# Performance work log

Hardware: AMD Instinct MI355X
Metric: run time of the kernel (lower is better)

## Reference

```python
import jax, jax.numpy as jnp
import numpy as np

B, IS, D = 16, 56, 768
NH, HD = 12, 64
WS = 14
MLP = 3072
EPS = 1e-5


def layer_norm(x, g, b):
    mu = jnp.mean(x, axis=-1, keepdims=True)
    var = jnp.mean(jnp.square(x - mu), axis=-1, keepdims=True)
    return (x - mu) * jax.lax.rsqrt(var + EPS) * g + b


def window_partition(x, ws):
    b, h, w, c = x.shape
    x = x.reshape(b, h // ws, ws, w // ws, ws, c)
    return x.transpose(0, 1, 3, 2, 4, 5).reshape(-1, ws, ws, c)


def window_unpartition(windows, ws, h, w, b):
    c = windows.shape[-1]
    x = windows.reshape(b, h // ws, w // ws, ws, ws, c)
    return x.transpose(0, 1, 3, 2, 4, 5).reshape(b, h, w, c)


def get_rel_pos(q_size, k_size, rel_pos):
    # q_size == k_size == WS here, table already has 2*WS-1 rows (no resize)
    coords = jnp.arange(q_size)[:, None] - jnp.arange(k_size)[None, :] + (k_size - 1)
    return rel_pos[coords]  # (q, k, hd)


def attention(x, qkv_w, qkv_b, proj_w, proj_b, rel_pos_h, rel_pos_w):
    b, h, w, d = x.shape
    scale = HD ** -0.5
    qkv = x @ qkv_w + qkv_b                                  # (b,h,w,3D)
    qkv = qkv.reshape(b, h * w, 3, NH, HD).transpose(2, 0, 3, 1, 4)
    qkv = qkv.reshape(3, b * NH, h * w, HD)
    q, k, v = qkv[0], qkv[1], qkv[2]
    attn = jnp.einsum('bqc,bkc->bqk', q * scale, k)          # (b*NH, hw, hw)
    # decomposed relative position bias
    rh = get_rel_pos(h, h, rel_pos_h)                        # (h,h,HD)
    rw = get_rel_pos(w, w, rel_pos_w)                        # (w,w,HD)
    r_q = q.reshape(b * NH, h, w, HD)
    rel_h = jnp.einsum('bhwc,hkc->bhwk', r_q, rh)
    rel_w = jnp.einsum('bhwc,wkc->bhwk', r_q, rw)
    attn = (attn.reshape(b * NH, h, w, h, w)
            + rel_h[:, :, :, :, None] + rel_w[:, :, :, None, :])
    attn = attn.reshape(b * NH, h * w, h * w)
    attn = jax.nn.softmax(attn, axis=-1)
    out = attn @ v                                           # (b*NH, hw, HD)
    out = out.reshape(b, NH, h, w, HD).transpose(0, 2, 3, 1, 4).reshape(b, h, w, d)
    return out @ proj_w + proj_b


def setup_inputs() -> dict:
    key = jax.random.key(0)
    ks = jax.random.split(key, 12)
    s = lambda fan_in: 1.0 / np.sqrt(fan_in)
    return {
        'x': jax.random.normal(ks[0], (B, IS, IS, D), jnp.float32),
        'norm1_g': jnp.ones((D,), jnp.float32),
        'norm1_b': jnp.zeros((D,), jnp.float32),
        'qkv_w': jax.random.normal(ks[1], (D, 3 * D), jnp.float32) * s(D),
        'qkv_b': jnp.zeros((3 * D,), jnp.float32),
        'proj_w': jax.random.normal(ks[2], (D, D), jnp.float32) * s(D),
        'proj_b': jnp.zeros((D,), jnp.float32),
        'rel_pos_h': jax.random.normal(ks[3], (2 * WS - 1, HD), jnp.float32) * 0.02,
        'rel_pos_w': jax.random.normal(ks[4], (2 * WS - 1, HD), jnp.float32) * 0.02,
        'norm2_g': jnp.ones((D,), jnp.float32),
        'norm2_b': jnp.zeros((D,), jnp.float32),
        'lin1_w': jax.random.normal(ks[5], (D, MLP), jnp.float32) * s(D),
        'lin1_b': jnp.zeros((MLP,), jnp.float32),
        'lin2_w': jax.random.normal(ks[6], (MLP, D), jnp.float32) * s(MLP),
        'lin2_b': jnp.zeros((D,), jnp.float32),
    }


def reference(x, norm1_g, norm1_b, qkv_w, qkv_b, proj_w, proj_b,
              rel_pos_h, rel_pos_w, norm2_g, norm2_b,
              lin1_w, lin1_b, lin2_w, lin2_b):
    b, h, w, d = x.shape
    shortcut = x
    xn = layer_norm(x, norm1_g, norm1_b)
    x_win = window_partition(xn, WS)
    attn_out = attention(x_win, qkv_w, qkv_b, proj_w, proj_b, rel_pos_h, rel_pos_w)
    attn_res = window_unpartition(attn_out, WS, h, w, b)
    hidden = shortcut + attn_res
    normed = layer_norm(hidden, norm2_g, norm2_b)
    m = jax.nn.gelu(normed.reshape(b, h * w, d) @ lin1_w + lin1_b, approximate=False)
    mlp_out = (m @ lin2_w + lin2_b).reshape(b, h, w, d)
    return hidden + mlp_out
```

## Files before the change

kernel.cpp:

```cpp
#include <hip/hip_runtime.h>
#include <cstdint>
#include <cstddef>


typedef unsigned short u16;
typedef __attribute__((ext_vector_type(8))) short bf16x8;
typedef __attribute__((ext_vector_type(4))) short bf16x4;
typedef __attribute__((ext_vector_type(4))) float f32x4;

#define MFMA16(a,b,c) __builtin_amdgcn_mfma_f32_16x16x32_bf16(a,b,c,0,0,0)

__device__ __forceinline__ float bf2f(u16 u){
  union { unsigned int i; float f; } v; v.i = ((unsigned int)u) << 16; return v.f;
}
__device__ __forceinline__ u16 f2bf(float f){
  union { float f; unsigned int i; } v; v.f = f;
  unsigned int r = v.i + 0x7FFFu + ((v.i >> 16) & 1u);
  return (u16)(r >> 16);
}
__device__ __forceinline__ f32x4 f4zero(){ f32x4 z; z[0]=z[1]=z[2]=z[3]=0.f; return z; }
__device__ __forceinline__ bf16x8 ld8(const u16* p){ return *reinterpret_cast<const bf16x8*>(p); }

__device__ __forceinline__ void gld_lds16(const u16* g, u16* l){
  __builtin_amdgcn_global_load_lds(
      (const __attribute__((address_space(1))) unsigned int*)(g),
      (__attribute__((address_space(3))) unsigned int*)(l), 16, 0, 0);
}

__global__ __launch_bounds__(256)
void conv_transpose(const float* __restrict__ in, u16* __restrict__ out, int R, int C)
{
  __shared__ float tile[32][33];
  int cb = C >> 5;
  int bx = blockIdx.x % cb, by = blockIdx.x / cb;
  int c0 = bx << 5, r0 = by << 5;
  int tx = threadIdx.x & 31, ty = threadIdx.x >> 5;
  #pragma unroll
  for (int k = 0; k < 4; k++)
    tile[ty + 8*k][tx] = in[(size_t)(r0 + ty + 8*k) * C + c0 + tx];
  __syncthreads();
  #pragma unroll
  for (int k = 0; k < 4; k++)
    out[(size_t)(c0 + ty + 8*k) * R + r0 + tx] = f2bf(tile[tx][ty + 8*k]);
}

__global__ __launch_bounds__(256)
void conv_bf16(const float* __restrict__ a, const float* __restrict__ b,
               u16* __restrict__ oa, u16* __restrict__ ob, int n)
{
  int i = blockIdx.x * 256 + threadIdx.x;
  if (i < n){ oa[i] = f2bf(a[i]); ob[i] = f2bf(b[i]); }
}

__global__ __launch_bounds__(256)
void ln_kernel(const float* __restrict__ in, const float* __restrict__ g,
               const float* __restrict__ b, u16* __restrict__ out, int window_map)
{
  const int wv = threadIdx.x >> 6, lane = threadIdx.x & 63;
  const int token = blockIdx.x * 4 + wv;
  const float* row = in + (size_t)token * 768;
  float vals[12];
  float s = 0.f, s2 = 0.f;
  #pragma unroll
  for (int j = 0; j < 3; j++){
    float4 u = *reinterpret_cast<const float4*>(row + j*256 + lane*4);
    float t[4] = {u.x, u.y, u.z, u.w};
    #pragma unroll
    for (int e = 0; e < 4; e++){ vals[j*4+e] = t[e]; s += t[e]; s2 += t[e]*t[e]; }
  }
  #pragma unroll
  for (int m = 1; m < 64; m <<= 1){ s += __shfl_xor(s, m, 64); s2 += __shfl_xor(s2, m, 64); }
  float mu  = s  * (1.f/768.f);
  float var = s2 * (1.f/768.f) - mu*mu;
  float rs  = rsqrtf(var + 1e-5f);
  size_t orow = (size_t)token;
  if (window_map){
    int b_ = token / 3136, rem = token % 3136;
    int hh = rem / 56, ww = rem % 56;
    int win = ((b_ << 2) + hh/14)*4 + ww/14;
    orow = (size_t)win * 196 + (hh%14)*14 + (ww%14);
  }
  u16* op = out + orow * 768;
  #pragma unroll
  for (int j = 0; j < 3; j++){
    int cb = j*256 + lane*4;
    float4 gg = *reinterpret_cast<const float4*>(g + cb);
    float4 bb = *reinterpret_cast<const float4*>(b + cb);
    float gt[4] = {gg.x, gg.y, gg.z, gg.w};
    float bt[4] = {bb.x, bb.y, bb.z, bb.w};
    bf16x4 o;
    #pragma unroll
    for (int e = 0; e < 4; e++)
      o[e] = (short)f2bf((vals[j*4+e] - mu) * rs * gt[e] + bt[e]);
    *reinterpret_cast<bf16x4*>(op + cb) = o;
  }
}

enum { EPI_QKV = 0, EPI_PROJ = 1, EPI_GELU = 2, EPI_MLP2 = 3 };

__global__ __launch_bounds__(256)
void gemm_bt(const u16* __restrict__ A, const u16* __restrict__ Bt,
             const float* __restrict__ bias, const float* __restrict__ residf,
             void* __restrict__ outp, int M, int N, int K, int epi)
{
  __shared__ __align__(16) u16 As[128][32];
  __shared__ __align__(16) u16 Bs[128][32];
  const int nb = N >> 7;
  const int bm = blockIdx.x / nb, bn = blockIdx.x % nb;
  const int m0 = bm << 7, n0 = bn << 7;
  const int tid = threadIdx.x;
  const int wv = tid >> 6, lane = tid & 63;
  const int wm = (wv & 1) << 6, wn = (wv >> 1) << 6;
  const int q = lane >> 4, c = lane & 15;

  f32x4 acc[4][4];
  #pragma unroll
  for (int i = 0; i < 4; i++)
    #pragma unroll
    for (int j = 0; j < 4; j++) acc[i][j] = f4zero();

  const int r0 = (wv << 5) + (lane >> 2);
  const int cq = (lane & 3) << 3;
  const u16* pa = A  + (size_t)(m0 + r0) * K + cq;
  const u16* pb = Bt + (size_t)(n0 + r0) * K + cq;
  const size_t skip = (size_t)16 * K;
  u16* lA0 = &As[wv << 5][0];
  u16* lA1 = &As[(wv << 5) + 16][0];
  u16* lB0 = &Bs[wv << 5][0];
  u16* lB1 = &Bs[(wv << 5) + 16][0];

  for (int k0 = 0; k0 < K; k0 += 32){
    gld_lds16(pa + k0,        lA0);
    gld_lds16(pa + skip + k0, lA1);
    gld_lds16(pb + k0,        lB0);
    gld_lds16(pb + skip + k0, lB1);
    __syncthreads();
    bf16x8 af[4], bfr[4];
    #pragma unroll
    for (int mi = 0; mi < 4; mi++) af[mi]  = ld8(&As[wm + mi*16 + c][q*8]);
    #pragma unroll
    for (int ni = 0; ni < 4; ni++) bfr[ni] = ld8(&Bs[wn + ni*16 + c][q*8]);
    #pragma unroll
    for (int mi = 0; mi < 4; mi++)
      #pragma unroll
      for (int ni = 0; ni < 4; ni++)
        acc[mi][ni] = MFMA16(af[mi], bfr[ni], acc[mi][ni]);
    __syncthreads();
  }

  #pragma unroll
  for (int mi = 0; mi < 4; mi++){
    #pragma unroll
    for (int r = 0; r < 4; r++){
      int grow = m0 + wm + mi*16 + q*4 + r;
      size_t orow = (size_t)grow;
      if (epi == EPI_PROJ){
        int win = grow / 196, loc = grow % 196;
        int b_ = win >> 4, wr = win & 15;
        int hh = (wr >> 2) * 14 + loc / 14;
        int ww = (wr & 3)  * 14 + loc % 14;
        orow = (size_t)((b_ * 56 + hh) * 56 + ww);
      }
      #pragma unroll
      for (int ni = 0; ni < 4; ni++){
        int col = n0 + wn + ni*16 + c;
        float v = acc[mi][ni][r] + bias[col];
        if (epi == EPI_PROJ){
          v += residf[orow * 768 + col];
          ((float*)outp)[orow * (size_t)N + col] = v;
        } else if (epi == EPI_MLP2){
          v += residf[(size_t)grow * 768 + col];
          ((float*)outp)[orow * (size_t)N + col] = v;
        } else {
          if (epi == EPI_GELU) v = 0.5f * v * (1.f + erff(v * 0.70710678f));
          ((u16*)outp)[orow * (size_t)N + col] = f2bf(v);
        }
      }
    }
  }
}

__global__ __launch_bounds__(256)
void attn_kernel(const u16* __restrict__ qkv, const u16* __restrict__ relh,
                 const u16* __restrict__ relw, u16* __restrict__ aout)
{
  __shared__ u16 Vt[64][232];
  __shared__ u16 P[4][16*216 + 16];
  __shared__ u16 RB[4][16][56];
  const int blk = blockIdx.x;
  const int win = blk / 12, head = blk % 12;
  const int tid = threadIdx.x;
  const int wv = tid >> 6, lane = tid & 63;
  const int q = lane >> 4, c = lane & 15;
  const u16* base = qkv + (size_t)win * 196 * 2304 + head * 64;

  for (int i = tid; i < 64*36; i += 256) Vt[i / 36][196 + i % 36] = 0;
  for (int i = tid; i < 4*144; i += 256){
    int w = i / 144, r = i % 144;
    int off = (r < 128) ? ((r >> 3) * 216 + 208 + (r & 7)) : (16*216 + (r - 128));
    P[w][off] = 0;
  }
  for (int i = tid; i < 196*8; i += 256){
    int t = i >> 3, h8 = (i & 7) << 3;
    bf16x8 v = ld8(base + (size_t)t * 2304 + 1536 + h8);
    #pragma unroll
    for (int j = 0; j < 8; j++) Vt[h8 + j][t] = (u16)v[j];
  }
  __syncthreads();

  const float scale = 0.125f;
  for (int mt = wv; mt < 13; mt += 4){
    const int m0 = mt * 16;
    int qr = m0 + c; if (qr > 195) qr = 195;
    const u16* qrow = base + (size_t)qr * 2304;
    bf16x8 aq0 = ld8(qrow + q*8);
    bf16x8 aq1 = ld8(qrow + 32 + q*8);

    f32x4 accs[13];
    #pragma unroll
    for (int nt = 0; nt < 13; nt++) accs[nt] = f4zero();
    #pragma unroll
    for (int nt = 0; nt < 13; nt++){
      int kt = nt*16 + c; if (kt > 195) kt = 195;
      const u16* krow = base + (size_t)kt * 2304 + 768;
      accs[nt] = MFMA16(aq0, ld8(krow + q*8), accs[nt]);
      accs[nt] = MFMA16(aq1, ld8(krow + 32 + q*8), accs[nt]);
    }

    f32x4 rha[2], rwa[2];
    #pragma unroll
    for (int ntt = 0; ntt < 2; ntt++){
      int dh = ntt*16 + c; if (dh > 26) dh = 26;
      const u16* ph = relh + dh*64;
      const u16* pw = relw + dh*64;
      rha[ntt] = MFMA16(aq0, ld8(ph + q*8), f4zero());
      rha[ntt] = MFMA16(aq1, ld8(ph + 32 + q*8), rha[ntt]);
      rwa[ntt] = MFMA16(aq0, ld8(pw + q*8), f4zero());
      rwa[ntt] = MFMA16(aq1, ld8(pw + 32 + q*8), rwa[ntt]);
    }
    #pragma unroll
    for (int ntt = 0; ntt < 2; ntt++)
      #pragma unroll
      for (int r = 0; r < 4; r++){
        int col = ntt*16 + c;
        if (col < 27){
          RB[wv][q*4+r][col]      = f2bf(rha[ntt][r]);
          RB[wv][q*4+r][28 + col] = f2bf(rwa[ntt][r]);
        }
      }

    #pragma unroll
    for (int r = 0; r < 4; r++){
      int it = m0 + q*4 + r; if (it > 195) it = 195;
      int hq = it / 14, wq = it % 14;
      float sv[13];
      float mx = -3e38f;
      #pragma unroll
      for (int nt = 0; nt < 13; nt++){
        int j = nt*16 + c;
        float x;
        if (j < 196){
          int hk = j / 14, wk = j % 14;
          x = accs[nt][r] * scale + bf2f(RB[wv][q*4+r][hq - hk + 13])
                                  + bf2f(RB[wv][q*4+r][28 + wq - wk + 13]);
        } else x = -3e38f;
        sv[nt] = x; mx = fmaxf(mx, x);
      }
      mx = fmaxf(mx, __shfl_xor(mx, 1, 64));
      mx = fmaxf(mx, __shfl_xor(mx, 2, 64));
      mx = fmaxf(mx, __shfl_xor(mx, 4, 64));
      mx = fmaxf(mx, __shfl_xor(mx, 8, 64));
      float sum = 0.f;
      #pragma unroll
      for (int nt = 0; nt < 13; nt++){ float p = __expf(sv[nt] - mx); sv[nt] = p; sum += p; }
      sum += __shfl_xor(sum, 1, 64); sum += __shfl_xor(sum, 2, 64);
      sum += __shfl_xor(sum, 4, 64); sum += __shfl_xor(sum, 8, 64);
      float is = 1.f / sum;
      #pragma unroll
      for (int nt = 0; nt < 13; nt++)
        P[wv][(q*4+r)*216 + nt*16 + c] = f2bf(sv[nt] * is);
    }

    f32x4 acco[4];
    #pragma unroll
    for (int nv = 0; nv < 4; nv++) acco[nv] = f4zero();
    #pragma unroll
    for (int ks = 0; ks < 7; ks++){
      bf16x8 ap = ld8(&P[wv][c*216 + ks*32 + q*8]);
      #pragma unroll
      for (int nv = 0; nv < 4; nv++){
        bf16x8 bv = ld8(&Vt[nv*16 + c][ks*32 + q*8]);
        acco[nv] = MFMA16(ap, bv, acco[nv]);
      }
    }
    #pragma unroll
    for (int nv = 0; nv < 4; nv++)
      #pragma unroll
      for (int r = 0; r < 4; r++){
        int it = m0 + q*4 + r;
        if (it < 196)
          aout[(size_t)(win*196 + it)*768 + head*64 + nv*16 + c] = f2bf(acco[nv][r]);
      }
  }
}

extern "C" void kernel_launch(void* const* d_in, const int* in_sizes, int n_in,
                              void* d_out, int out_size, void* d_ws, size_t ws_size,
                              hipStream_t stream)
{
  (void)in_sizes; (void)n_in; (void)out_size; (void)ws_size;
  const float* x      = (const float*)d_in[0];
  const float* n1g    = (const float*)d_in[1];
  const float* n1b    = (const float*)d_in[2];
  const float* qkv_w  = (const float*)d_in[3];
  const float* qkv_b  = (const float*)d_in[4];
  const float* proj_w = (const float*)d_in[5];
  const float* proj_b = (const float*)d_in[6];
  const float* relh   = (const float*)d_in[7];
  const float* relw   = (const float*)d_in[8];
  const float* n2g    = (const float*)d_in[9];
  const float* n2b    = (const float*)d_in[10];
  const float* lin1_w = (const float*)d_in[11];
  const float* lin1_b = (const float*)d_in[12];
  const float* lin2_w = (const float*)d_in[13];
  const float* lin2_b = (const float*)d_in[14];
  float* out = (float*)d_out;

  char* ws = (char*)d_ws;
  u16* qkvwt  = (u16*)(ws);
  u16* projwt = (u16*)(ws +  3538944);
  u16* lin1wt = (u16*)(ws +  4718592);
  u16* lin2wt = (u16*)(ws +  9437184);
  u16* relhb  = (u16*)(ws + 14155776);
  u16* relwb  = (u16*)(ws + 14159232);
  u16* bufA   = (u16*)(ws + 14162688);
  u16* bufQ   = (u16*)(ws + 14162688 + (size_t)77070336);

  conv_transpose<<<(768/32)*(2304/32), 256, 0, stream>>>(qkv_w,  qkvwt, 768, 2304);
  conv_transpose<<<(768/32)*(768/32),  256, 0, stream>>>(proj_w, projwt, 768, 768);
  conv_transpose<<<(768/32)*(3072/32), 256, 0, stream>>>(lin1_w, lin1wt, 768, 3072);
  conv_transpose<<<(3072/32)*(768/32), 256, 0, stream>>>(lin2_w, lin2wt, 3072, 768);
  conv_bf16<<<(27*64 + 255)/256, 256, 0, stream>>>(relh, relw, relhb, relwb, 27*64);

  ln_kernel<<<12544, 256, 0, stream>>>(x, n1g, n1b, bufA, 1);
  gemm_bt<<<392*18, 256, 0, stream>>>(bufA, qkvwt, qkv_b, nullptr, bufQ,
                                      50176, 2304, 768, EPI_QKV);
  attn_kernel<<<3072, 256, 0, stream>>>(bufQ, relhb, relwb, bufA);
  gemm_bt<<<392*6, 256, 0, stream>>>(bufA, projwt, proj_b, x, out,
                                     50176, 768, 768, EPI_PROJ);
  ln_kernel<<<12544, 256, 0, stream>>>(out, n2g, n2b, bufA, 0);
  for (int h = 0; h < 2; h++){
    const u16* nrm = bufA + (size_t)h * 25088 * 768;
    float* hid     = out  + (size_t)h * 25088 * 768;
    gemm_bt<<<196*24, 256, 0, stream>>>(nrm, lin1wt, lin1_b, nullptr, bufQ,
                                        25088, 3072, 768, EPI_GELU);
    gemm_bt<<<196*6, 256, 0, stream>>>(bufQ, lin2wt, lin2_b, hid, hid,
                                       25088, 768, 3072, EPI_MLP2);
  }
}
```

Before: 2.271 ms.

## Replace 128x128 GEMM with double-buffered 256x256 tile kernel using swizzled LDS

Swaps the single-buffered 128x128x32 bf16 GEMM for a 512-thread 256x256x64 tile kernel. It double-buffers global-to-LDS loads with explicit vmcnt waits, applies an XOR swizzle to LDS rows to avoid bank conflicts, interleaves MFMA quadrants with setprio and scheduling barriers, and remaps block IDs across the XCDs. The aim is more operand reuse per tile, with load latency hidden behind compute. In exchange it uses more registers and LDS per block and relies on hand-written wait counts, and with 256-wide tiles the N=768 GEMMs launch few blocks.

New measurement: 2.495 ms. 1.1x slower.

```diff
diff --git a/kernel.cpp b/kernel.cpp
--- a/kernel.cpp
+++ b/kernel.cpp
@@ -26,6 +26,14 @@
       (const __attribute__((address_space(1))) unsigned int*)(g),
       (__attribute__((address_space(3))) unsigned int*)(l), 16, 0, 0);
 }
+
+#define BAR   __builtin_amdgcn_s_barrier()
+#define SB0   __builtin_amdgcn_sched_barrier(0)
+#define PRIO1 __builtin_amdgcn_s_setprio(1)
+#define PRIO0 __builtin_amdgcn_s_setprio(0)
+#define VM8   asm volatile("s_waitcnt vmcnt(8)" ::: "memory")
+#define VM0   asm volatile("s_waitcnt vmcnt(0)" ::: "memory")
+#define LGKM0 asm volatile("s_waitcnt lgkmcnt(0)" ::: "memory")
 
 __global__ __launch_bounds__(256)
 void conv_transpose(const float* __restrict__ in, u16* __restrict__ out, int R, int C)
@@ -98,61 +106,112 @@
 
 enum { EPI_QKV = 0, EPI_PROJ = 1, EPI_GELU = 2, EPI_MLP2 = 3 };
 
-__global__ __launch_bounds__(256)
-void gemm_bt(const u16* __restrict__ A, const u16* __restrict__ Bt,
+__global__ __launch_bounds__(512, 2)
+void gemm256(const u16* __restrict__ A, const u16* __restrict__ Bt,
              const float* __restrict__ bias, const float* __restrict__ residf,
              void* __restrict__ outp, int M, int N, int K, int epi)
 {
-  __shared__ __align__(16) u16 As[128][32];
-  __shared__ __align__(16) u16 Bs[128][32];
-  const int nb = N >> 7;
-  const int bm = blockIdx.x / nb, bn = blockIdx.x % nb;
-  const int m0 = bm << 7, n0 = bn << 7;
+  __shared__ u16 lds[2][2][16384];
+  const int nbn = N >> 8;
+  const int nwg = gridDim.x;
+  const int orig = blockIdx.x;
+  const int qq = nwg >> 3, rr = nwg & 7;
+  const int xcd = orig & 7, idx = orig >> 3;
+  const int wg = (xcd < rr ? xcd*(qq+1) : rr*(qq+1) + (xcd-rr)*qq) + idx;
+  const int bm = wg / nbn, bn = wg % nbn;
+  const int m0 = bm << 8, n0 = bn << 8;
   const int tid = threadIdx.x;
   const int wv = tid >> 6, lane = tid & 63;
-  const int wm = (wv & 1) << 6, wn = (wv >> 1) << 6;
   const int q = lane >> 4, c = lane & 15;
-
-  f32x4 acc[4][4];
-  #pragma unroll
-  for (int i = 0; i < 4; i++)
+  const int wmI = wv >> 2, wnI = wv & 3;
+
+  f32x4 acc[8][4];
+  #pragma unroll
+  for (int i = 0; i < 8; i++)
     #pragma unroll
     for (int j = 0; j < 4; j++) acc[i][j] = f4zero();
 
-  const int r0 = (wv << 5) + (lane >> 2);
-  const int cq = (lane & 3) << 3;
-  const u16* pa = A  + (size_t)(m0 + r0) * K + cq;
-  const u16* pb = Bt + (size_t)(n0 + r0) * K + cq;
-  const size_t skip = (size_t)16 * K;
-  u16* lA0 = &As[wv << 5][0];
-  u16* lA1 = &As[(wv << 5) + 16][0];
-  u16* lB0 = &Bs[wv << 5][0];
-  u16* lB1 = &Bs[(wv << 5) + 16][0];
-
-  for (int k0 = 0; k0 < K; k0 += 32){
-    gld_lds16(pa + k0,        lA0);
-    gld_lds16(pa + skip + k0, lA1);
-    gld_lds16(pb + k0,        lB0);
-    gld_lds16(pb + skip + k0, lB1);
-    __syncthreads();
-    bf16x8 af[4], bfr[4];
-    #pragma unroll
-    for (int mi = 0; mi < 4; mi++) af[mi]  = ld8(&As[wm + mi*16 + c][q*8]);
-    #pragma unroll
-    for (int ni = 0; ni < 4; ni++) bfr[ni] = ld8(&Bs[wn + ni*16 + c][q*8]);
-    #pragma unroll
-    for (int mi = 0; mi < 4; mi++)
-      #pragma unroll
-      for (int ni = 0; ni < 4; ni++)
-        acc[mi][ni] = MFMA16(af[mi], bfr[ni], acc[mi][ni]);
-    __syncthreads();
-  }
-
-  #pragma unroll
-  for (int mi = 0; mi < 4; mi++){
+  int offA[2][2], offB[2][2];
+  #pragma unroll
+  for (int j = 0; j < 2; j++){
+    int p = ((wv*2 + j) << 10) + lane*16;
+    int b = p ^ (((p >> 7) & 7) << 4);
+    int brow = b >> 7;
+    int bcol = (b & 127) >> 1;
+    #pragma unroll
+    for (int h = 0; h < 2; h++){
+      offA[j][h] = (m0 + h*128 + brow) * K + bcol;
+      offB[j][h] = (n0 + h*128 + brow) * K + bcol;
+    }
+  }
+
+  #define STAGE(BB, T) do {                                              \
+    int ko_ = (T) << 6;                                                  \
+    _Pragma("unroll") for (int j_ = 0; j_ < 2; j_++)                     \
+    _Pragma("unroll") for (int h_ = 0; h_ < 2; h_++){                    \
+      gld_lds16(A  + offA[j_][h_] + ko_,                                 \
+                &lds[BB][0][h_*8192 + (wv*2 + j_)*512]);                 \
+      gld_lds16(Bt + offB[j_][h_] + ko_,                                 \
+                &lds[BB][1][h_*8192 + (wv*2 + j_)*512]);                 \
+    }                                                                    \
+  } while(0)
+
+  const int rA0 = wmI*128 + c;
+  const int rB0 = wnI*64 + c;
+  const int xb[2] = { (q*16) ^ ((c & 7) << 4), (64 + q*16) ^ ((c & 7) << 4) };
+
+  #define RD_A(BB, MH, I, KS)                                            \
+    af[I][KS] = ld8((const u16*)((const char*)&lds[BB][0][0] +           \
+                    (((rA0 + (MH)*64 + (I)*16) << 7) + xb[KS])))
+  #define RD_B0(BB, NN, KS)                                              \
+    bq0[NN][KS] = ld8((const u16*)((const char*)&lds[BB][1][0] +         \
+                    (((rB0 + (NN)*16) << 7) + xb[KS])))
+  #define RD_B1(BB, NN, KS)                                              \
+    bq1[NN][KS] = ld8((const u16*)((const char*)&lds[BB][1][0] +         \
+                    (((rB0 + 32 + (NN)*16) << 7) + xb[KS])))
+
+  #define MMQ(MH, NH, BQ)                                                \
+    _Pragma("unroll") for (int i_ = 0; i_ < 4; i_++)                     \
+    _Pragma("unroll") for (int n_ = 0; n_ < 2; n_++)                     \
+    _Pragma("unroll") for (int k_ = 0; k_ < 2; k_++)                     \
+      acc[(MH)*4+i_][(NH)*2+n_] =                                        \
+        MFMA16(af[i_][k_], BQ[n_][k_], acc[(MH)*4+i_][(NH)*2+n_])
+
+  bf16x8 af[4][2], bq0[2][2], bq1[2][2];
+
+  #define TILE4(BB) do {                                                 \
+    _Pragma("unroll") for (int i_ = 0; i_ < 4; i_++){                    \
+      RD_A(BB, 0, i_, 0); RD_A(BB, 0, i_, 1); }                          \
+    _Pragma("unroll") for (int n_ = 0; n_ < 2; n_++){                    \
+      RD_B0(BB, n_, 0); RD_B0(BB, n_, 1); }                              \
+    BAR; LGKM0; SB0; PRIO1; MMQ(0,0,bq0); PRIO0; BAR; SB0;               \
+    _Pragma("unroll") for (int n_ = 0; n_ < 2; n_++){                    \
+      RD_B1(BB, n_, 0); RD_B1(BB, n_, 1); }                              \
+    BAR; LGKM0; SB0; PRIO1; MMQ(0,1,bq1); PRIO0; BAR; SB0;               \
+    _Pragma("unroll") for (int i_ = 0; i_ < 4; i_++){                    \
+      RD_A(BB, 1, i_, 0); RD_A(BB, 1, i_, 1); }                          \
+    BAR; LGKM0; SB0; PRIO1; MMQ(1,0,bq0); PRIO0; BAR; SB0;               \
+    PRIO1; MMQ(1,1,bq1); PRIO0; BAR; SB0;                                \
+  } while(0)
+
+  const int nT = K >> 6;
+  STAGE(0, 0); STAGE(1, 1);
+  VM8; BAR; SB0;
+  for (int t = 0; t < nT; t += 2){
+    TILE4(0);
+    if (t + 2 < nT){ STAGE(0, t+2); VM8; } else { VM0; }
+    BAR; SB0;
+    TILE4(1);
+    if (t + 3 < nT){ STAGE(1, t+3); VM8; BAR; SB0; }
+  }
+
+  const int mrow0 = m0 + wmI*128;
+  const int ncol0 = n0 + wnI*64;
+  #pragma unroll
+  for (int mi = 0; mi < 8; mi++){
     #pragma unroll
     for (int r = 0; r < 4; r++){
-      int grow = m0 + wm + mi*16 + q*4 + r;
+      int grow = mrow0 + mi*16 + q*4 + r;
       size_t orow = (size_t)grow;
       if (epi == EPI_PROJ){
         int win = grow / 196, loc = grow % 196;
@@ -163,7 +222,7 @@
       }
       #pragma unroll
       for (int ni = 0; ni < 4; ni++){
-        int col = n0 + wn + ni*16 + c;
+        int col = ncol0 + ni*16 + c;
         float v = acc[mi][ni][r] + bias[col];
         if (epi == EPI_PROJ){
           v += residf[orow * 768 + col];
@@ -178,6 +237,12 @@
       }
     }
   }
+  #undef STAGE
+  #undef RD_A
+  #undef RD_B0
+  #undef RD_B1
+  #undef MMQ
+  #undef TILE4
 }
 
 __global__ __launch_bounds__(256)
@@ -343,18 +408,18 @@
   conv_bf16<<<(27*64 + 255)/256, 256, 0, stream>>>(relh, relw, relhb, relwb, 27*64);
 
   ln_kernel<<<12544, 256, 0, stream>>>(x, n1g, n1b, bufA, 1);
-  gemm_bt<<<392*18, 256, 0, stream>>>(bufA, qkvwt, qkv_b, nullptr, bufQ,
-                                      50176, 2304, 768, EPI_QKV);
+  gemm256<<<196*9, 512, 0, stream>>>(bufA, qkvwt, qkv_b, nullptr, bufQ,
+                                     50176, 2304, 768, EPI_QKV);
   attn_kernel<<<3072, 256, 0, stream>>>(bufQ, relhb, relwb, bufA);
-  gemm_bt<<<392*6, 256, 0, stream>>>(bufA, projwt, proj_b, x, out,
+  gemm256<<<196*3, 512, 0, stream>>>(bufA, projwt, proj_b, x, out,
                                      50176, 768, 768, EPI_PROJ);
   ln_kernel<<<12544, 256, 0, stream>>>(out, n2g, n2b, bufA, 0);
   for (int h = 0; h < 2; h++){
     const u16* nrm = bufA + (size_t)h * 25088 * 768;
     float* hid     = out  + (size_t)h * 25088 * 768;
-    gemm_bt<<<196*24, 256, 0, stream>>>(nrm, lin1wt, lin1_b, nullptr, bufQ,
-                                        25088, 3072, 768, EPI_GELU);
-    gemm_bt<<<196*6, 256, 0, stream>>>(bufQ, lin2wt, lin2_b, hid, hid,
-                                       25088, 768, 3072, EPI_MLP2);
-  }
-}
+    gemm256<<<98*12, 512, 0, stream>>>(nrm, lin1wt, lin1_b, nullptr, bufQ,
+                                       25088, 3072, 768, EPI_GELU);
+    gemm256<<<98*3, 512, 0, stream>>>(bufQ, lin2wt, lin2_b, hid, hid,
+                                      25088, 768, 3072, EPI_MLP2);
+  }
+}
```
